# Kernel tuning notes

Measured on AMD Instinct MI355X. Metric: run time of the kernel, lower is better.

## Reference

```python
import jax, jax.numpy as jnp
import numpy as np

B, N, IN, E, OUT = 4, 128, 256, 128, 128
EPS = 1e-5
NEG = -1.0e9


def _ln(x, s, o):
    m = x.mean(-1, keepdims=True)
    v = ((x - m) ** 2).mean(-1, keepdims=True)
    return s * jax.lax.rsqrt(v + EPS) * (x - m) + o


def setup_inputs() -> dict:
    key = jax.random.key(0)
    ks = jax.random.split(key, 30)

    def w(k, i, o):
        return (jax.random.normal(k, (i, o), jnp.float32) / np.sqrt(i)).astype(jnp.float32)

    z_dense = jax.random.normal(ks[0], (B, N, IN), jnp.float32)
    e_dense = jax.random.normal(ks[1], (B, N, N, E), jnp.float32)
    graph_fts = jax.random.normal(ks[2], (B, IN // 2), jnp.float32)
    lengths = jax.random.randint(ks[3], (B,), N // 2, N + 1)
    mask = jnp.arange(N)[None, :] < lengths[:, None]  # (B,N) bool
    adj = jax.random.uniform(ks[4], (B, N, N)) < 0.3
    adj = (adj | jnp.eye(N, dtype=bool)[None]) & mask[:, :, None] & mask[:, None, :]
    return dict(
        z_dense=z_dense, e_dense=e_dense, graph_fts=graph_fts, mask=mask, adj_mat=adj,
        Wt1=w(ks[5], IN, 8), Wt2=w(ks[6], IN, 8), Wt3=w(ks[7], IN, 8),
        We1=w(ks[8], E, 8), We2=w(ks[9], E, 8), We3=w(ks[10], E, 8),
        Wg=w(ks[11], IN // 2, 8),
        Wm1=w(ks[12], IN, OUT), Wm2=w(ks[13], IN, OUT), Wme=w(ks[14], E, OUT), Wmg=w(ks[15], E, OUT),
        ln1_s=jnp.ones((OUT,), jnp.float32), ln1_o=jnp.zeros((OUT,), jnp.float32),
        Wmlp1=w(ks[16], OUT, OUT),
        ln2_s=jnp.ones((OUT,), jnp.float32), ln2_o=jnp.zeros((OUT,), jnp.float32),
        Wmlp2=w(ks[17], OUT, OUT),
        WU1=w(ks[18], IN, OUT), WU2=w(ks[19], OUT, OUT), WU3=w(ks[20], 8, OUT),
        lnf_s=jnp.ones((OUT,), jnp.float32), lnf_o=jnp.zeros((OUT,), jnp.float32),
    )


def reference(z_dense, e_dense, graph_fts, mask, adj_mat,
              Wt1, Wt2, Wt3, We1, We2, We3, Wg,
              Wm1, Wm2, Wme, Wmg,
              ln1_s, ln1_o, Wmlp1, ln2_s, ln2_o, Wmlp2,
              WU1, WU2, WU3, lnf_s, lnf_o):
    mN = mask[..., None]  # (B,N,1)
    # --- triplet messages ---
    tri_1 = jnp.where(mN, z_dense @ Wt1, 0.0)  # (B,N,8)
    tri_2 = jnp.where(mN, z_dense @ Wt2, 0.0)
    tri_3 = jnp.where(mN, z_dense @ Wt3, 0.0)
    tri_e1 = e_dense @ We1  # (B,N,N,8)
    tri_e2 = e_dense @ We2
    tri_e3 = e_dense @ We3
    tri_g = graph_fts @ Wg  # (B,8)
    # (B,N,N,N,8) 7-way broadcast sum (axes: b, i, j, k)
    tri = (tri_1[:, :, None, None, :] + tri_2[:, None, :, None, :] + tri_3[:, None, None, :, :]
           + tri_e1[:, :, :, None, :] + tri_e2[:, :, None, :, :] + tri_e3[:, None, :, :, :]
           + tri_g[:, None, None, None, :])
    msk_tri = mask[:, None, None, :] | mask[:, None, :, None] | mask[:, :, None, None]
    tri = jnp.where(msk_tri[..., None], tri, NEG)
    tri_pooled = tri.max(axis=1)  # (B,N,N,8) -- max over first node axis
    tri_msgs = jax.nn.relu(tri_pooled @ WU3)  # (B,N,N,OUT)

    # --- pairwise messages ---
    msg_1 = jnp.where(mN, z_dense @ Wm1, 0.0)  # (B,N,OUT)
    msg_2 = jnp.where(mN, z_dense @ Wm2, 0.0)
    msg_e = jnp.where(adj_mat[..., None], e_dense @ Wme, 0.0)  # (B,N,N,OUT)
    msg_g = graph_fts @ Wmg  # (B,OUT)
    msgs = msg_1[:, None, :, :] + msg_2[:, :, None, :] + msg_e + msg_g[:, None, None, :]
    # M[-1]: [LN, ReLU, Linear] x2
    x = jax.nn.relu(_ln(msgs, ln1_s, ln1_o)) @ Wmlp1
    x = jax.nn.relu(_ln(x, ln2_s, ln2_o)) @ Wmlp2
    msgs = jnp.where(adj_mat[..., None], x, NEG).max(axis=1)  # (B,N,OUT)

    ret = _ln(z_dense @ WU1 + msgs @ WU2, lnf_s, lnf_o)  # (B,N,OUT)
    return ret, msgs, tri_msgs
```

## Files before the change

kernel.cpp:

```cpp
#include <hip/hip_runtime.h>

#define BN   4
#define NN   128
#define INF  256
#define EF   128
#define OUTF 128
#define EPSF 1e-5f
#define NEGF -998244352.0f

typedef __attribute__((ext_vector_type(8))) short short8;
typedef __attribute__((ext_vector_type(4))) float f32x4;

#define MFMA16(a, b, c) __builtin_amdgcn_mfma_f32_16x16x32_bf16(a, b, c, 0, 0, 0)

__device__ __forceinline__ unsigned short f2bf(float f) {
    unsigned u = __float_as_uint(f);
    u += 0x7fffu + ((u >> 16) & 1u);
    return (unsigned short)(u >> 16);
}
__device__ __forceinline__ unsigned pack2(float a, float b) {
    return (unsigned)f2bf(a) | ((unsigned)f2bf(b) << 16);
}

constexpr size_t TRI1 = 0;
constexpr size_t TRI2 = 4096;
constexpr size_t TRI3 = 8192;
constexpr size_t MSG1 = 12288;
constexpr size_t MSG2 = 77824;
constexpr size_t ZWU1 = 143360;
constexpr size_t TRIG = 208896;
constexpr size_t MSGG = 209920;
constexpr size_t E1T  = 210944;
constexpr size_t E2T  = 735232;
constexpr size_t E3N  = 1259520;
constexpr size_t PREPF = 1783808;

constexpr int W1T_OFF  = 0;
constexpr int W2T_OFF  = 16384;
constexpr int WMET_OFF = 32768;

constexpr size_t O_RET = 0;
constexpr size_t O_MSG = 65536;
constexpr size_t O_TRI = 131072;

__device__ __forceinline__ int detect_int(const void* mask) {
    const unsigned char* m = (const unsigned char*)mask;
    return (m[1] | m[2] | m[3]) == 0 ? 1 : 0;
}
__device__ __forceinline__ bool rdbool(const void* p, size_t idx, int isInt) {
    if (isInt) return ((const int*)p)[idx] != 0;
    return ((const unsigned char*)p)[idx] != 0;
}

__global__ __launch_bounds__(256, 4) void k_pre(
    const float* __restrict__ z, const float* __restrict__ e, const void* __restrict__ mask,
    const float* __restrict__ Wt1, const float* __restrict__ Wt2, const float* __restrict__ Wt3,
    const float* __restrict__ Wm1, const float* __restrict__ Wm2, const float* __restrict__ WU1,
    const float* __restrict__ g, const float* __restrict__ Wg, const float* __restrict__ Wmg,
    const float* __restrict__ W1, const float* __restrict__ W2, const float* __restrict__ Wme,
    const float* __restrict__ We1, const float* __restrict__ We2, const float* __restrict__ We3,
    float* __restrict__ ws, unsigned short* __restrict__ prep)
{
    int bx = blockIdx.x, tid = threadIdx.x;
    __shared__ __align__(16) unsigned char smem[128 * 136 * 2];

    if (bx < 512) {
        unsigned short* Ab = (unsigned short*)smem;
        int bi = bx;
        int b = bi >> 7, i = bi & 127;
        int lane = tid & 63, w = tid >> 6, q = lane >> 4, n = lane & 15;
        {
            int half = lane >> 5, c4 = (lane & 31) * 4;
            #pragma unroll
            for (int it = 0; it < 16; it++) {
                int row = 32 * w + 2 * it + half;
                float4 v = *(const float4*)(e + (size_t)bi * 16384 + (size_t)row * 128 + c4);
                unsigned* dst = (unsigned*)&Ab[row * 136 + c4];
                dst[0] = pack2(v.x, v.y);
                dst[1] = pack2(v.z, v.w);
            }
        }
        short8 bfrag[4][2];
        {
            int colbase = n;
            #pragma unroll
            for (int t = 0; t < 2; t++) {
                int col = 16 * t + colbase;
                const float* Wsel = (col < 8) ? We1 : (col < 16 ? We2 : We3);
                int csel = col & 7;
                float mval = (col < 24) ? 1.f : 0.f;
                #pragma unroll
                for (int ks = 0; ks < 4; ks++) {
                    union { short8 s; unsigned short u[8]; } tmp;
                    #pragma unroll
                    for (int jj = 0; jj < 8; jj++) {
                        int k = ks * 32 + q * 8 + jj;
                        tmp.u[jj] = f2bf(Wsel[k * 8 + csel] * mval);
                    }
                    bfrag[ks][t] = tmp.s;
                }
            }
        }
        __builtin_amdgcn_wave_barrier();

        f32x4 ac2[2][2];
        #pragma unroll
        for (int rt = 0; rt < 2; rt++)
            #pragma unroll
            for (int t = 0; t < 2; t++) ac2[rt][t] = 0.f;
        #pragma unroll
        for (int ks = 0; ks < 4; ks++) {
            int k0 = ks * 32 + q * 8;
            short8 a0 = *(const short8*)&Ab[(32 * w + n) * 136 + k0];
            short8 a1 = *(const short8*)&Ab[(32 * w + 16 + n) * 136 + k0];
            #pragma unroll
            for (int t = 0; t < 2; t++) {
                ac2[0][t] = MFMA16(a0, bfrag[ks][t], ac2[0][t]);
                ac2[1][t] = MFMA16(a1, bfrag[ks][t], ac2[1][t]);
            }
        }
        #pragma unroll
        for (int rt = 0; rt < 2; rt++)
            #pragma unroll
            for (int reg = 0; reg < 4; reg++) {
                int row = 32 * w + 16 * rt + 4 * q + reg;
                float v0 = ac2[rt][0][reg];
                if (n < 8) ws[E1T + ((size_t)(b * 128 + row) * 128 + i) * 8 + n] = v0;
                else       ws[E2T + ((size_t)(b * 128 + row) * 128 + i) * 8 + (n - 8)] = v0;
                if (n < 8) ws[E3N + ((size_t)bi * 128 + row) * 8 + n] = ac2[rt][1][reg];
            }
        return;
    }
    if (bx < 1024) {
        int bn = bx - 512;
        int isInt = detect_int(mask);
        float* zr = (float*)smem;
        zr[tid] = z[(size_t)bn * INF + tid];
        __syncthreads();
        float mk = rdbool(mask, bn, isInt) ? 1.f : 0.f;
        for (int idx = tid; idx < 408; idx += 256) {
            const float* W; int c; size_t dst; int width; bool msk;
            if (idx < 8)        { W = Wt1; c = idx;       dst = TRI1 + (size_t)bn * 8;   width = 8;   msk = true;  }
            else if (idx < 16)  { W = Wt2; c = idx - 8;   dst = TRI2 + (size_t)bn * 8;   width = 8;   msk = true;  }
            else if (idx < 24)  { W = Wt3; c = idx - 16;  dst = TRI3 + (size_t)bn * 8;   width = 8;   msk = true;  }
            else if (idx < 152) { W = Wm1; c = idx - 24;  dst = MSG1 + (size_t)bn * 128; width = 128; msk = true;  }
            else if (idx < 280) { W = Wm2; c = idx - 152; dst = MSG2 + (size_t)bn * 128; width = 128; msk = true;  }
            else                { W = WU1; c = idx - 280; dst = ZWU1 + (size_t)bn * 128; width = 128; msk = false; }
            float acc = 0.f;
            #pragma unroll 8
            for (int k = 0; k < INF; k++) acc += zr[k] * W[k * width + c];
            ws[dst + c] = msk ? acc * mk : acc;
        }
        return;
    }
    if (bx < 1028) {
        int b = bx - 1024;
        float* gr = (float*)smem;
        if (tid < 128) gr[tid] = g[b * 128 + tid];
        __syncthreads();
        if (tid < 8) {
            float a = 0.f;
            for (int k = 0; k < 128; k++) a += gr[k] * Wg[k * 8 + tid];
            ws[TRIG + b * 8 + tid] = a;
        } else if (tid >= 128) {
            int c = tid - 128;
            float a = 0.f;
            for (int k = 0; k < 128; k++) a += gr[k] * Wmg[k * 128 + c];
            ws[MSGG + b * 128 + c] = a;
        }
        return;
    }
    {
        int idx = (bx - 1028) * 256 + tid;
        const float* W = (idx < 16384) ? W1 : (idx < 32768 ? W2 : Wme);
        int local = idx & 16383;
        int f = local >> 3, jj = local & 7;
        int lane = f & 63, fg = f >> 6;
        int t = fg & 7, ks = fg >> 3;
        int n = lane & 15, q = lane >> 4;
        int row = 16 * t + n;
        int k = ks * 32 + q * 8 + jj;
        prep[idx] = f2bf(W[k * 128 + row]);
    }
}

constexpr int PSTR2 = 264;
constexpr int QSTR2 = 268;

__global__ __launch_bounds__(256, 4) void k_main(
    const float* __restrict__ e, const void* __restrict__ mask, const void* __restrict__ adj,
    const float* __restrict__ ln1s, const float* __restrict__ ln1o,
    const float* __restrict__ ln2s, const float* __restrict__ ln2o,
    const unsigned short* __restrict__ prep, const float* __restrict__ WU3,
    float* __restrict__ ws, float* __restrict__ out)
{
    int bx = blockIdx.x, tid = threadIdx.x;
    int gct = bx / 3, r3 = bx - gct * 3;
    __shared__ __align__(16) unsigned char smem[128 * 136 * 2 + 2048];
    int lane = tid & 63, w = tid >> 6, q = lane >> 4, n = lane & 15;

    if (r3 == 2) {
        int g = gct;
        int j0 = ((g >> 3) & 7) * 16, k0 = (g & 7) * 16, b = g >> 6;
        int isInt = detect_int(mask);
        float* Pl = (float*)smem;
        float* Ql = (float*)(smem + 16 * PSTR2 * 4);
        float* pooled = Pl;
        float* WU3l   = Ql;
        __shared__ unsigned char mloc[128];

        if (tid < 128) mloc[tid] = rdbool(mask, b * 128 + tid, isInt) ? 1 : 0;

        int tj = tid >> 4, tk = tid & 15;
        int sr = tid >> 4, seg = tid & 15;
        float accM[8], accU[8];
        #pragma unroll
        for (int c = 0; c < 8; c++) { accM[c] = NEGF; accU[c] = NEGF; }

        for (int i0 = 0; i0 < 128; i0 += 32) {
            __syncthreads();
            {
                const float4* e1 = (const float4*)(ws + E1T + (size_t)(b * 128 + j0 + sr) * 1024 + i0 * 8 + seg * 16);
                const float4* t1 = (const float4*)(ws + TRI1 + (size_t)b * 1024 + i0 * 8 + seg * 16);
                const float4* e2 = (const float4*)(ws + E2T + (size_t)(b * 128 + k0 + sr) * 1024 + i0 * 8 + seg * 16);
                float* pd = Pl + sr * PSTR2 + seg * 16;
                float* qd = Ql + sr * QSTR2 + seg * 16;
                #pragma unroll
                for (int t = 0; t < 4; t++) {
                    float4 a = e1[t], bb = t1[t], qv = e2[t];
                    pd[t * 4 + 0] = a.x + bb.x; pd[t * 4 + 1] = a.y + bb.y;
                    pd[t * 4 + 2] = a.z + bb.z; pd[t * 4 + 3] = a.w + bb.w;
                    qd[t * 4 + 0] = qv.x; qd[t * 4 + 1] = qv.y;
                    qd[t * 4 + 2] = qv.z; qd[t * 4 + 3] = qv.w;
                }
            }
            __syncthreads();
            const float* pp = Pl + tj * PSTR2;
            const float* qq = Ql + tk * QSTR2;
            for (int ii = 0; ii < 32; ii++) {
                bool m_i = mloc[i0 + ii] != 0;
                float4 p0 = *(const float4*)(pp + ii * 8);
                float4 p1 = *(const float4*)(pp + ii * 8 + 4);
                float4 q0 = *(const float4*)(qq + ii * 8);
                float4 q1 = *(const float4*)(qq + ii * 8 + 4);
                float v[8] = { p0.x + q0.x, p0.y + q0.y, p0.z + q0.z, p0.w + q0.w,
                               p1.x + q1.x, p1.y + q1.y, p1.z + q1.z, p1.w + q1.w };
                if (m_i) {
                    #pragma unroll
                    for (int c = 0; c < 8; c++) accM[c] = fmaxf(accM[c], v[c]);
                } else {
                    #pragma unroll
                    for (int c = 0; c < 8; c++) accU[c] = fmaxf(accU[c], v[c]);
                }
            }
        }
        float sel[8];
        {
            bool all_i = (mloc[j0 + tj] | mloc[k0 + tk]) != 0;
            #pragma unroll
            for (int c = 0; c < 8; c++) sel[c] = all_i ? fmaxf(accM[c], accU[c]) : accM[c];
        }
        __syncthreads();
        {
            const float* t2 = ws + TRI2 + (size_t)(b * 128 + j0 + tj) * 8;
            const float* t3 = ws + TRI3 + (size_t)(b * 128 + k0 + tk) * 8;
            const float* e3 = ws + E3N + ((size_t)(b * 128 + j0 + tj) * 128 + (k0 + tk)) * 8;
            const float* tg = ws + TRIG + (size_t)b * 8;
            #pragma unroll
            for (int c = 0; c < 8; c++)
                pooled[tid * 8 + c] = sel[c] + t2[c] + t3[c] + e3[c] + tg[c];
            *(float4*)(WU3l + tid * 4) = *(const float4*)(WU3 + tid * 4);
        }
        __syncthreads();
        int col4 = (tid & 31) * 4, rowgrp = tid >> 5;
        #pragma unroll
        for (int pass = 0; pass < 32; pass++) {
            int p = pass * 8 + rowgrp;
            const float* pl = pooled + p * 8;
            float4 s = { 0.f, 0.f, 0.f, 0.f };
            #pragma unroll
            for (int c = 0; c < 8; c++) {
                float pv = pl[c];
                float4 wv = *(const float4*)(WU3l + c * 128 + col4);
                s.x += pv * wv.x; s.y += pv * wv.y; s.z += pv * wv.z; s.w += pv * wv.w;
            }
            s.x = fmaxf(s.x, 0.f); s.y = fmaxf(s.y, 0.f);
            s.z = fmaxf(s.z, 0.f); s.w = fmaxf(s.w, 0.f);
            int pj = p >> 4, pk = p & 15;
            *(float4*)(out + O_TRI + ((size_t)(b * 128 + j0 + pj) * 128 + (k0 + pk)) * 128 + col4) = s;
        }
        return;
    }

    unsigned short* Ab = (unsigned short*)smem;
    float* pw = (float*)(smem + 128 * 136 * 2);
    int bj = gct * 2 + r3;
    int b = bj >> 7, j = bj & 127;
    int isInt = detect_int(mask);

    {
        int half = lane >> 5, c4 = (lane & 31) * 4;
        #pragma unroll
        for (int it = 0; it < 16; it++) {
            int row = 32 * w + 2 * it + half;
            float4 v = *(const float4*)(e + (((size_t)b * 128 + row) * 128 + j) * 128 + c4);
            unsigned* dst = (unsigned*)&Ab[row * 136 + c4];
            dst[0] = pack2(v.x, v.y);
            dst[1] = pack2(v.z, v.w);
        }
    }
    __builtin_amdgcn_wave_barrier();

    f32x4 acc[2][8];
    #pragma unroll
    for (int rt = 0; rt < 2; rt++)
        #pragma unroll
        for (int t = 0; t < 8; t++) acc[rt][t] = 0.f;

    #pragma unroll
    for (int ks = 0; ks < 4; ks++) {
        int k0 = ks * 32 + q * 8;
        short8 a0 = *(const short8*)&Ab[(32 * w + n) * 136 + k0];
        short8 a1 = *(const short8*)&Ab[(32 * w + 16 + n) * 136 + k0];
        #pragma unroll
        for (int t = 0; t < 8; t++) {
            short8 bt = *(const short8*)&prep[WMET_OFF + ((ks * 8 + t) * 64 + lane) * 8];
            acc[0][t] = MFMA16(a0, bt, acc[0][t]);
            acc[1][t] = MFMA16(a1, bt, acc[1][t]);
        }
    }

    float msum[8];
    #pragma unroll
    for (int t = 0; t < 8; t++)
        msum[t] = ws[MSG1 + (size_t)bj * 128 + 16 * t + n] + ws[MSGG + (size_t)b * 128 + 16 * t + n];
    float adjm[2][4];
    float rs[2][4], rss[2][4];
    #pragma unroll
    for (int rt = 0; rt < 2; rt++)
        #pragma unroll
        for (int reg = 0; reg < 4; reg++) {
            int row = 32 * w + 16 * rt + 4 * q + reg;
            bool av = rdbool(adj, ((size_t)b * 128 + row) * 128 + j, isInt);
            adjm[rt][reg] = av ? 1.f : 0.f;
            float s = 0.f, ssq = 0.f;
            #pragma unroll
            for (int t = 0; t < 8; t++) {
                float v = acc[rt][t][reg] * adjm[rt][reg]
                        + ws[MSG2 + ((size_t)b * 128 + row) * 128 + 16 * t + n] + msum[t];
                acc[rt][t][reg] = v;
                s += v; ssq += v * v;
            }
            rs[rt][reg] = s; rss[rt][reg] = ssq;
        }
    #pragma unroll
    for (int d = 1; d < 16; d <<= 1) {
        #pragma unroll
        for (int rt = 0; rt < 2; rt++)
            #pragma unroll
            for (int reg = 0; reg < 4; reg++) {
                rs[rt][reg]  += __shfl_xor(rs[rt][reg], d, 64);
                rss[rt][reg] += __shfl_xor(rss[rt][reg], d, 64);
            }
    }
    {
        float s1v[8], o1v[8];
        #pragma unroll
        for (int t = 0; t < 8; t++) { s1v[t] = ln1s[16 * t + n]; o1v[t] = ln1o[16 * t + n]; }
        #pragma unroll
        for (int rt = 0; rt < 2; rt++)
            #pragma unroll
            for (int reg = 0; reg < 4; reg++) {
                float mu = rs[rt][reg] * (1.f / 128);
                float inv = rsqrtf(rss[rt][reg] * (1.f / 128) - mu * mu + EPSF);
                int row = 32 * w + 16 * rt + 4 * q + reg;
                #pragma unroll
                for (int t = 0; t < 8; t++) {
                    float v = fmaxf(s1v[t] * inv * (acc[rt][t][reg] - mu) + o1v[t], 0.f);
                    Ab[row * 136 + 16 * t + n] = f2bf(v);
                }
            }
    }
    __builtin_amdgcn_wave_barrier();

    #pragma unroll
    for (int rt = 0; rt < 2; rt++)
        #pragma unroll
        for (int t = 0; t < 8; t++) acc[rt][t] = 0.f;
    #pragma unroll
    for (int ks = 0; ks < 4; ks++) {
        int k0 = ks * 32 + q * 8;
        short8 a0 = *(const short8*)&Ab[(32 * w + n) * 136 + k0];
        short8 a1 = *(const short8*)&Ab[(32 * w + 16 + n) * 136 + k0];
        #pragma unroll
        for (int t = 0; t < 8; t++) {
            short8 bt = *(const short8*)&prep[W1T_OFF + ((ks * 8 + t) * 64 + lane) * 8];
            acc[0][t] = MFMA16(a0, bt, acc[0][t]);
            acc[1][t] = MFMA16(a1, bt, acc[1][t]);
        }
    }
    #pragma unroll
    for (int rt = 0; rt < 2; rt++)
        #pragma unroll
        for (int reg = 0; reg < 4; reg++) {
            float s = 0.f, ssq = 0.f;
            #pragma unroll
            for (int t = 0; t < 8; t++) { float v = acc[rt][t][reg]; s += v; ssq += v * v; }
            rs[rt][reg] = s; rss[rt][reg] = ssq;
        }
    #pragma unroll
    for (int d = 1; d < 16; d <<= 1) {
        #pragma unroll
        for (int rt = 0; rt < 2; rt++)
            #pragma unroll
            for (int reg = 0; reg < 4; reg++) {
                rs[rt][reg]  += __shfl_xor(rs[rt][reg], d, 64);
                rss[rt][reg] += __shfl_xor(rss[rt][reg], d, 64);
            }
    }
    {
        float s2v[8], o2v[8];
        #pragma unroll
        for (int t = 0; t < 8; t++) { s2v[t] = ln2s[16 * t + n]; o2v[t] = ln2o[16 * t + n]; }
        #pragma unroll
        for (int rt = 0; rt < 2; rt++)
            #pragma unroll
            for (int reg = 0; reg < 4; reg++) {
                float mu = rs[rt][reg] * (1.f / 128);
                float inv = rsqrtf(rss[rt][reg] * (1.f / 128) - mu * mu + EPSF);
                int row = 32 * w + 16 * rt + 4 * q + reg;
                #pragma unroll
                for (int t = 0; t < 8; t++) {
                    float v = fmaxf(s2v[t] * inv * (acc[rt][t][reg] - mu) + o2v[t], 0.f);
                    Ab[row * 136 + 16 * t + n] = f2bf(v);
                }
            }
    }
    __builtin_amdgcn_wave_barrier();

    #pragma unroll
    for (int rt = 0; rt < 2; rt++)
        #pragma unroll
        for (int t = 0; t < 8; t++) acc[rt][t] = 0.f;
    #pragma unroll
    for (int ks = 0; ks < 4; ks++) {
        int k0 = ks * 32 + q * 8;
        short8 a0 = *(const short8*)&Ab[(32 * w + n) * 136 + k0];
        short8 a1 = *(const short8*)&Ab[(32 * w + 16 + n) * 136 + k0];
        #pragma unroll
        for (int t = 0; t < 8; t++) {
            short8 bt = *(const short8*)&prep[W2T_OFF + ((ks * 8 + t) * 64 + lane) * 8];
            acc[0][t] = MFMA16(a0, bt, acc[0][t]);
            acc[1][t] = MFMA16(a1, bt, acc[1][t]);
        }
    }
    float colmax[8];
    #pragma unroll
    for (int t = 0; t < 8; t++) colmax[t] = NEGF;
    #pragma unroll
    for (int rt = 0; rt < 2; rt++)
        #pragma unroll
        for (int reg = 0; reg < 4; reg++) {
            if (adjm[rt][reg] > 0.f) {
                #pragma unroll
                for (int t = 0; t < 8; t++) colmax[t] = fmaxf(colmax[t], acc[rt][t][reg]);
            }
        }
    #pragma unroll
    for (int t = 0; t < 8; t++) {
        colmax[t] = fmaxf(colmax[t], __shfl_xor(colmax[t], 16, 64));
        colmax[t] = fmaxf(colmax[t], __shfl_xor(colmax[t], 32, 64));
    }
    if (lane < 16) {
        #pragma unroll
        for (int t = 0; t < 8; t++) pw[w * 128 + 16 * t + lane] = colmax[t];
    }
    __syncthreads();
    if (tid < 128) {
        float mx = fmaxf(fmaxf(pw[tid], pw[128 + tid]), fmaxf(pw[256 + tid], pw[384 + tid]));
        out[O_MSG + (size_t)bj * 128 + tid] = mx;
    }
}

__global__ __launch_bounds__(128) void k_final(
    const float* __restrict__ ws, const float* __restrict__ WU2,
    const float* __restrict__ lnfs, const float* __restrict__ lnfo,
    float* __restrict__ out)
{
    int bn = blockIdx.x, tid = threadIdx.x;
    __shared__ float mrow[128];
    __shared__ float red[4];
    mrow[tid] = out[O_MSG + (size_t)bn * 128 + tid];
    __syncthreads();
    float y = ws[ZWU1 + (size_t)bn * 128 + tid];
    #pragma unroll 8
    for (int k = 0; k < 128; k++) y += mrow[k] * WU2[k * 128 + tid];
    float s = y, ss = y * y;
    for (int d = 1; d < 64; d <<= 1) { s += __shfl_xor(s, d, 64); ss += __shfl_xor(ss, d, 64); }
    if ((tid & 63) == 0) { red[(tid >> 6) * 2] = s; red[(tid >> 6) * 2 + 1] = ss; }
    __syncthreads();
    float S = red[0] + red[2], SS = red[1] + red[3];
    float m_ = S * (1.f / 128), v_ = SS * (1.f / 128) - m_ * m_;
    float r = rsqrtf(v_ + EPSF);
    out[O_RET + (size_t)bn * 128 + tid] = lnfs[tid] * r * (y - m_) + lnfo[tid];
}

extern "C" void kernel_launch(void* const* d_in, const int* in_sizes, int n_in,
                              void* d_out, int out_size, void* d_ws, size_t ws_size,
                              hipStream_t stream)
{
    const float* z    = (const float*)d_in[0];
    const float* e    = (const float*)d_in[1];
    const float* gf   = (const float*)d_in[2];
    const void*  mask = d_in[3];
    const void*  adj  = d_in[4];
    const float* Wt1 = (const float*)d_in[5];
    const float* Wt2 = (const float*)d_in[6];
    const float* Wt3 = (const float*)d_in[7];
    const float* We1 = (const float*)d_in[8];
    const float* We2 = (const float*)d_in[9];
    const float* We3 = (const float*)d_in[10];
    const float* Wg  = (const float*)d_in[11];
    const float* Wm1 = (const float*)d_in[12];
    const float* Wm2 = (const float*)d_in[13];
    const float* Wme = (const float*)d_in[14];
    const float* Wmg = (const float*)d_in[15];
    const float* ln1s = (const float*)d_in[16];
    const float* ln1o = (const float*)d_in[17];
    const float* W1   = (const float*)d_in[18];
    const float* ln2s = (const float*)d_in[19];
    const float* ln2o = (const float*)d_in[20];
    const float* W2   = (const float*)d_in[21];
    const float* WU1  = (const float*)d_in[22];
    const float* WU2  = (const float*)d_in[23];
    const float* WU3  = (const float*)d_in[24];
    const float* lnfs = (const float*)d_in[25];
    const float* lnfo = (const float*)d_in[26];
    float* out = (float*)d_out;
    float* ws  = (float*)d_ws;
    unsigned short* prep = (unsigned short*)(ws + PREPF);

    hipLaunchKernelGGL(k_pre, dim3(1220), dim3(256), 0, stream,
                       z, e, mask, Wt1, Wt2, Wt3, Wm1, Wm2, WU1, gf, Wg, Wmg,
                       W1, W2, Wme, We1, We2, We3, ws, prep);
    hipLaunchKernelGGL(k_main, dim3(768), dim3(256), 0, stream,
                       e, mask, adj, ln1s, ln1o, ln2s, ln2o, prep, WU3, ws, out);
    hipLaunchKernelGGL(k_final, dim3(512), dim3(128), 0, stream,
                       ws, WU2, lnfs, lnfo, out);
}
```

Baseline: 209.6 us.

## Store E1/E2 triplet edge projections as bf16 and stage full i-range in LDS

The edge-projection stage now writes the E1T and E2T intermediates as bf16 instead of fp32, halving their global traffic. The triplet-pooling blocks load the whole 128-wide i range of P (E1+T1, repacked to bf16) and Q into LDS once, with a single barrier, instead of looping over four 32-wide chunks with two barriers each. The inner max loop unpacks the bf16 pairs to fp32 before adding. The cost is reduced precision in the triplet max inputs (bf16 rounding of E1, E2 and of P after adding T1) and a different LDS layout.

Result: slower. 217.1 us (+3.6%).

```diff
diff --git a/kernel.cpp b/kernel.cpp
--- a/kernel.cpp
+++ b/kernel.cpp
@@ -82,10 +82,9 @@
         }
         short8 bfrag[4][2];
         {
-            int colbase = n;
             #pragma unroll
             for (int t = 0; t < 2; t++) {
-                int col = 16 * t + colbase;
+                int col = 16 * t + n;
                 const float* Wsel = (col < 8) ? We1 : (col < 16 ? We2 : We3);
                 int csel = col & 7;
                 float mval = (col < 24) ? 1.f : 0.f;
@@ -119,14 +118,16 @@
                 ac2[1][t] = MFMA16(a1, bfrag[ks][t], ac2[1][t]);
             }
         }
+        unsigned short* e1t = (unsigned short*)(ws + E1T);
+        unsigned short* e2t = (unsigned short*)(ws + E2T);
         #pragma unroll
         for (int rt = 0; rt < 2; rt++)
             #pragma unroll
             for (int reg = 0; reg < 4; reg++) {
                 int row = 32 * w + 16 * rt + 4 * q + reg;
                 float v0 = ac2[rt][0][reg];
-                if (n < 8) ws[E1T + ((size_t)(b * 128 + row) * 128 + i) * 8 + n] = v0;
-                else       ws[E2T + ((size_t)(b * 128 + row) * 128 + i) * 8 + (n - 8)] = v0;
+                if (n < 8) e1t[((size_t)(b * 128 + row) * 128 + i) * 8 + n] = f2bf(v0);
+                else       e2t[((size_t)(b * 128 + row) * 128 + i) * 8 + (n - 8)] = f2bf(v0);
                 if (n < 8) ws[E3N + ((size_t)bi * 128 + row) * 8 + n] = ac2[rt][1][reg];
             }
         return;
@@ -184,9 +185,6 @@
     }
 }
 
-constexpr int PSTR2 = 264;
-constexpr int QSTR2 = 268;
-
 __global__ __launch_bounds__(256, 4) void k_main(
     const float* __restrict__ e, const void* __restrict__ mask, const void* __restrict__ adj,
     const float* __restrict__ ln1s, const float* __restrict__ ln1o,
@@ -203,48 +201,65 @@
         int g = gct;
         int j0 = ((g >> 3) & 7) * 16, k0 = (g & 7) * 16, b = g >> 6;
         int isInt = detect_int(mask);
-        float* Pl = (float*)smem;
-        float* Ql = (float*)(smem + 16 * PSTR2 * 4);
-        float* pooled = Pl;
-        float* WU3l   = Ql;
+        unsigned short* Pl = (unsigned short*)smem;
+        unsigned short* Ql = (unsigned short*)(smem + 16 * 528 * 2);
+        float* pooled = (float*)smem;
+        float* WU3l   = (float*)(smem + 8192);
         __shared__ unsigned char mloc[128];
-
         if (tid < 128) mloc[tid] = rdbool(mask, b * 128 + tid, isInt) ? 1 : 0;
 
+        const unsigned short* e1t = (const unsigned short*)(ws + E1T);
+        const unsigned short* e2t = (const unsigned short*)(ws + E2T);
+        {
+            float t1v[2][8];
+            #pragma unroll
+            for (int h = 0; h < 2; h++) {
+                const float* t1p = ws + TRI1 + (size_t)b * 1024 + h * 512 + lane * 8;
+                #pragma unroll
+                for (int x = 0; x < 8; x++) t1v[h][x] = t1p[x];
+            }
+            #pragma unroll
+            for (int r4 = 0; r4 < 4; r4++) {
+                int row = 4 * w + r4;
+                #pragma unroll
+                for (int h = 0; h < 2; h++) {
+                    int pos = h * 512 + lane * 8;
+                    short8 qv = *(const short8*)&e2t[(size_t)(b * 128 + k0 + row) * 1024 + pos];
+                    *(short8*)&Ql[row * 536 + pos] = qv;
+                    short8 ev = *(const short8*)&e1t[(size_t)(b * 128 + j0 + row) * 1024 + pos];
+                    union { short8 s; unsigned u[4]; } ou;
+                    #pragma unroll
+                    for (int x = 0; x < 4; x++) {
+                        unsigned d = ((const unsigned*)&ev)[x];
+                        float lo = __uint_as_float(d << 16)         + t1v[h][2 * x];
+                        float hi = __uint_as_float(d & 0xffff0000u) + t1v[h][2 * x + 1];
+                        ou.u[x] = pack2(lo, hi);
+                    }
+                    *(short8*)&Pl[row * 528 + pos] = ou.s;
+                }
+            }
+        }
+        __syncthreads();
+
         int tj = tid >> 4, tk = tid & 15;
-        int sr = tid >> 4, seg = tid & 15;
         float accM[8], accU[8];
         #pragma unroll
         for (int c = 0; c < 8; c++) { accM[c] = NEGF; accU[c] = NEGF; }
-
-        for (int i0 = 0; i0 < 128; i0 += 32) {
-            __syncthreads();
-            {
-                const float4* e1 = (const float4*)(ws + E1T + (size_t)(b * 128 + j0 + sr) * 1024 + i0 * 8 + seg * 16);
-                const float4* t1 = (const float4*)(ws + TRI1 + (size_t)b * 1024 + i0 * 8 + seg * 16);
-                const float4* e2 = (const float4*)(ws + E2T + (size_t)(b * 128 + k0 + sr) * 1024 + i0 * 8 + seg * 16);
-                float* pd = Pl + sr * PSTR2 + seg * 16;
-                float* qd = Ql + sr * QSTR2 + seg * 16;
-                #pragma unroll
-                for (int t = 0; t < 4; t++) {
-                    float4 a = e1[t], bb = t1[t], qv = e2[t];
-                    pd[t * 4 + 0] = a.x + bb.x; pd[t * 4 + 1] = a.y + bb.y;
-                    pd[t * 4 + 2] = a.z + bb.z; pd[t * 4 + 3] = a.w + bb.w;
-                    qd[t * 4 + 0] = qv.x; qd[t * 4 + 1] = qv.y;
-                    qd[t * 4 + 2] = qv.z; qd[t * 4 + 3] = qv.w;
+        {
+            const unsigned short* pp = &Pl[tj * 528];
+            const unsigned short* qq = &Ql[tk * 536];
+            for (int ii = 0; ii < 128; ii++) {
+                bool m_i = mloc[ii] != 0;
+                short8 pv = *(const short8*)&pp[ii * 8];
+                short8 qv = *(const short8*)&qq[ii * 8];
+                float v[8];
+                #pragma unroll
+                for (int x = 0; x < 4; x++) {
+                    unsigned dp = ((const unsigned*)&pv)[x];
+                    unsigned dq = ((const unsigned*)&qv)[x];
+                    v[2 * x]     = __uint_as_float(dp << 16)         + __uint_as_float(dq << 16);
+                    v[2 * x + 1] = __uint_as_float(dp & 0xffff0000u) + __uint_as_float(dq & 0xffff0000u);
                 }
-            }
-            __syncthreads();
-            const float* pp = Pl + tj * PSTR2;
-            const float* qq = Ql + tk * QSTR2;
-            for (int ii = 0; ii < 32; ii++) {
-                bool m_i = mloc[i0 + ii] != 0;
-                float4 p0 = *(const float4*)(pp + ii * 8);
-                float4 p1 = *(const float4*)(pp + ii * 8 + 4);
-                float4 q0 = *(const float4*)(qq + ii * 8);
-                float4 q1 = *(const float4*)(qq + ii * 8 + 4);
-                float v[8] = { p0.x + q0.x, p0.y + q0.y, p0.z + q0.z, p0.w + q0.w,
-                               p1.x + q1.x, p1.y + q1.y, p1.z + q1.z, p1.w + q1.w };
                 if (m_i) {
                     #pragma unroll
                     for (int c = 0; c < 8; c++) accM[c] = fmaxf(accM[c], v[c]);
```
